# Kernel optimization log

Hardware: AMD Instinct MI355X
Metric: run time of the kernel (lower is better)

Reference implementation:

```python
import jax, jax.numpy as jnp
import numpy as np

B, E, N, F = 8, 2048, 2048, 128

def setup_inputs() -> dict:
    key = jax.random.key(0)
    k1, k2, k3, k4 = jax.random.split(key, 4)
    node_embeddings = jax.random.normal(k1, (B, N, F), dtype=jnp.float32)
    adj = jax.random.randint(k2, (B, E, N), -1, 3).astype(jnp.float32)
    W = jax.random.normal(k3, (F, F), dtype=jnp.float32) * (1.0 / np.sqrt(F))
    b = jax.random.normal(k4, (F,), dtype=jnp.float32) * 0.01
    return {"node_embeddings": node_embeddings, "adj": adj, "W": W, "b": b}

def reference(node_embeddings, adj, W, b):
    # adj_target: 1 where adj == -1, else 0
    adj_target = (adj == -1).astype(node_embeddings.dtype)          # [B, E, N]
    norm = jnp.sum(adj_target, axis=-1, keepdims=True)               # [B, E, 1]
    norm = jnp.where(norm == 0, 1.0, norm)
    # masked-mean aggregation of neighbor vertices into hyperedges
    message_vertex = jnp.matmul(adj_target, node_embeddings) / norm  # [B, E, F]
    # linear (torch Linear: x @ W.T + b) + relu
    hyperedge_embeddings = jax.nn.relu(jnp.matmul(message_vertex, W.T) + b)
    return hyperedge_embeddings
```

## Files before the change

### kernel.cpp

```cpp
#include <hip/hip_runtime.h>
#include <hip/hip_bf16.h>

#define B_ 8
#define E_ 2048
#define N_ 2048
#define F_ 128

#define BM 64
#define MT 4
#define BK 64
#define MP 136

using bf16x8 = __bf16 __attribute__((ext_vector_type(8)));
using fx4    = float __attribute__((ext_vector_type(4)));

__global__ __launch_bounds__(256) void prep_all(const float* __restrict__ node,
                                                const float* __restrict__ W,
                                                __bf16* __restrict__ nodeT,
                                                __bf16* __restrict__ Wb) {
    const int bid = blockIdx.x;
    const int t   = threadIdx.x;

    if (bid < 512) {
        const int b  = bid & 7;
        const int n0 = (bid >> 3) * 32;
        const int f  = t & 127;
        const int nb = n0 + (t >> 7) * 16;
        const float* src = node + ((size_t)b * N_ + nb) * F_ + f;
        __bf16 h[16];
#pragma unroll
        for (int i = 0; i < 16; ++i)
            h[i] = (__bf16)src[(size_t)i * F_];
        __bf16* dst = nodeT + ((size_t)b * F_ + f) * N_ + nb;
        *(uint4*)&dst[0] = *(const uint4*)&h[0];
        *(uint4*)&dst[8] = *(const uint4*)&h[8];
    } else {
        int idx = (bid - 512) * 256 + t;
        float4 v = *(const float4*)&W[idx * 4];
        __bf16 o[4] = {(__bf16)v.x, (__bf16)v.y, (__bf16)v.z, (__bf16)v.w};
        *(uint2*)&Wb[idx * 4] = *(const uint2*)o;
    }
}

__global__ __launch_bounds__(256, 1) void v2h_main(const float* __restrict__ adj,
                                                   const __bf16* __restrict__ nodeT,
                                                   const __bf16* __restrict__ Wb,
                                                   const float* __restrict__ bias,
                                                   float* __restrict__ out) {
    __shared__ __align__(16) __bf16 Bs[2][128][64];
    __shared__ __align__(16) unsigned long long Abits[2][64];
    __shared__ __align__(16) float normS[BM];
    __shared__ __align__(16) __bf16 Ms[BM * MP];

    const int t    = threadIdx.x;
    const int bid  = blockIdx.x;
    const int b    = bid & 7;
    const int e0   = (bid >> 3) * BM;
    const int w    = t >> 6;
    const int lane = t & 63;
    const int l15  = lane & 15;
    const int quad = lane >> 4;

    const int ar   = lane >> 2;
    const int acs  = lane & 3;
    const int arow = w * 16 + ar;
    const float* aPtr = adj + ((size_t)b * E_ + e0 + arow) * N_ + acs * 16;

    const __bf16* nTB = nodeT + (size_t)b * F_ * N_;

    auto issue_dma = [&](int k0, int buf) {
#pragma unroll
        for (int p = 0; p < 4; ++p) {
            int idx = t + 256 * p;
            int f   = idx >> 3;
            int sl  = idx & 7;
            int g   = sl ^ (f & 7);
            const __bf16* src = nTB + (size_t)f * N_ + k0 + g * 8;
            __bf16* dst = &Bs[buf][0][0] + (size_t)(w * 64 + 256 * p) * 8;
            __builtin_amdgcn_global_load_lds(
                (const __attribute__((address_space(1))) void*)src,
                (__attribute__((address_space(3))) void*)dst, 16, 0, 0);
        }
    };

    auto cvt16 = [](float4 v0, float4 v1, float4 v2, float4 v3) -> unsigned {
        unsigned m = 0;
        m |= (v0.x == -1.f) ? 1u     : 0u;
        m |= (v0.y == -1.f) ? 2u     : 0u;
        m |= (v0.z == -1.f) ? 4u     : 0u;
        m |= (v0.w == -1.f) ? 8u     : 0u;
        m |= (v1.x == -1.f) ? 16u    : 0u;
        m |= (v1.y == -1.f) ? 32u    : 0u;
        m |= (v1.z == -1.f) ? 64u    : 0u;
        m |= (v1.w == -1.f) ? 128u   : 0u;
        m |= (v2.x == -1.f) ? 256u   : 0u;
        m |= (v2.y == -1.f) ? 512u   : 0u;
        m |= (v2.z == -1.f) ? 1024u  : 0u;
        m |= (v2.w == -1.f) ? 2048u  : 0u;
        m |= (v3.x == -1.f) ? 4096u  : 0u;
        m |= (v3.y == -1.f) ? 8192u  : 0u;
        m |= (v3.z == -1.f) ? 16384u : 0u;
        m |= (v3.w == -1.f) ? 32768u : 0u;
        return m;
    };

    auto unpack = [](unsigned byte) -> bf16x8 {
        union { unsigned u[4]; bf16x8 v; } r;
        r.u[0] = ((byte &   1u) ? 0x3F80u : 0u) | ((byte &   2u) ? 0x3F800000u : 0u);
        r.u[1] = ((byte &   4u) ? 0x3F80u : 0u) | ((byte &   8u) ? 0x3F800000u : 0u);
        r.u[2] = ((byte &  16u) ? 0x3F80u : 0u) | ((byte &  32u) ? 0x3F800000u : 0u);
        r.u[3] = ((byte &  64u) ? 0x3F80u : 0u) | ((byte & 128u) ? 0x3F800000u : 0u);
        return r.v;
    };

    fx4 acc[MT][2] = {};
    int cnt = 0;

    float4 a0 = *(const float4*)(aPtr + 0);
    float4 a1 = *(const float4*)(aPtr + 4);
    float4 a2 = *(const float4*)(aPtr + 8);
    float4 a3 = *(const float4*)(aPtr + 12);
    issue_dma(0, 0);
    {
        unsigned bits = cvt16(a0, a1, a2, a3);
        ((unsigned short*)&Abits[0][arow])[acs] = (unsigned short)bits;
        cnt += __popc(bits);
    }
    a0 = *(const float4*)(aPtr + BK + 0);
    a1 = *(const float4*)(aPtr + BK + 4);
    a2 = *(const float4*)(aPtr + BK + 8);
    a3 = *(const float4*)(aPtr + BK + 12);

#pragma unroll
    for (int m = 0; m < 32; ++m) {
        const int buf = m & 1;
        __syncthreads();

        if (m < 31)
            issue_dma((m + 1) * BK, buf ^ 1);
        if (m < 31) {
            unsigned bits = cvt16(a0, a1, a2, a3);
            ((unsigned short*)&Abits[buf ^ 1][arow])[acs] = (unsigned short)bits;
            cnt += __popc(bits);
        }
        if (m < 30) {
            const float* ap = aPtr + (m + 2) * BK;
            a0 = *(const float4*)(ap + 0);
            a1 = *(const float4*)(ap + 4);
            a2 = *(const float4*)(ap + 8);
            a3 = *(const float4*)(ap + 12);
        }

        bf16x8 af0[MT], af1[MT];
#pragma unroll
        for (int mt = 0; mt < MT; ++mt) {
            unsigned long long v = Abits[buf][mt * 16 + l15];
            unsigned lo = (unsigned)v, hi = (unsigned)(v >> 32);
            af0[mt] = unpack((lo >> (8 * quad)) & 255u);
            af1[mt] = unpack((hi >> (8 * quad)) & 255u);
        }

#pragma unroll
        for (int ft = 0; ft < 2; ++ft) {
            int f  = w * 32 + ft * 16 + l15;
            int q0 = quad ^ (f & 7);
            int q1 = (4 + quad) ^ (f & 7);
            bf16x8 b0 = *(const bf16x8*)&Bs[buf][f][q0 * 8];
#pragma unroll
            for (int mt = 0; mt < MT; ++mt)
                acc[mt][ft] = __builtin_amdgcn_mfma_f32_16x16x32_bf16(af0[mt], b0, acc[mt][ft], 0, 0, 0);
            bf16x8 b1 = *(const bf16x8*)&Bs[buf][f][q1 * 8];
#pragma unroll
            for (int mt = 0; mt < MT; ++mt)
                acc[mt][ft] = __builtin_amdgcn_mfma_f32_16x16x32_bf16(af1[mt], b1, acc[mt][ft], 0, 0, 0);
        }
    }

    {
        float c = (float)cnt;
        c += __shfl_xor(c, 1);
        c += __shfl_xor(c, 2);
        if (acs == 0)
            normS[arow] = 1.f / fmaxf(c, 1.f);
    }
    __syncthreads();

    const int rbase = quad * 4;
    float4 rn[MT];
#pragma unroll
    for (int mt = 0; mt < MT; ++mt)
        rn[mt] = *(const float4*)&normS[mt * 16 + rbase];

#pragma unroll
    for (int ft = 0; ft < 2; ++ft) {
        int fcol = w * 32 + ft * 16 + l15;
#pragma unroll
        for (int mt = 0; mt < MT; ++mt) {
            const float* rr = (const float*)&rn[mt];
#pragma unroll
            for (int r = 0; r < 4; ++r)
                Ms[(mt * 16 + rbase + r) * MP + fcol] = (__bf16)(acc[mt][ft][r] * rr[r]);
        }
    }
    __syncthreads();

    fx4 acc2[MT][2] = {};
#pragma unroll
    for (int ks = 0; ks < 4; ++ks) {
        bf16x8 afm[MT];
#pragma unroll
        for (int mt = 0; mt < MT; ++mt)
            afm[mt] = *(const bf16x8*)&Ms[(mt * 16 + l15) * MP + ks * 32 + quad * 8];
#pragma unroll
        for (int gt = 0; gt < 2; ++gt) {
            int g = w * 32 + gt * 16 + l15;
            bf16x8 wfr = *(const bf16x8*)&Wb[(size_t)g * F_ + ks * 32 + quad * 8];
#pragma unroll
            for (int mt = 0; mt < MT; ++mt)
                acc2[mt][gt] = __builtin_amdgcn_mfma_f32_16x16x32_bf16(afm[mt], wfr, acc2[mt][gt], 0, 0, 0);
        }
    }

#pragma unroll
    for (int gt = 0; gt < 2; ++gt) {
        int g = w * 32 + gt * 16 + l15;
        float bb = bias[g];
#pragma unroll
        for (int mt = 0; mt < MT; ++mt) {
#pragma unroll
            for (int r = 0; r < 4; ++r) {
                int e = e0 + mt * 16 + rbase + r;
                float v = acc2[mt][gt][r] + bb;
                out[((size_t)b * E_ + e) * F_ + g] = fmaxf(v, 0.f);
            }
        }
    }
}

extern "C" void kernel_launch(void* const* d_in, const int* in_sizes, int n_in,
                              void* d_out, int out_size, void* d_ws, size_t ws_size,
                              hipStream_t stream) {
    const float* node = (const float*)d_in[0];
    const float* adj  = (const float*)d_in[1];
    const float* W    = (const float*)d_in[2];
    const float* bias = (const float*)d_in[3];
    float* out = (float*)d_out;

    char* ws = (char*)d_ws;
    __bf16* nodeT = (__bf16*)ws;
    __bf16* Wb    = (__bf16*)(ws + 8 * 1024 * 1024);

    prep_all<<<528, 256, 0, stream>>>(node, W, nodeT, Wb);
    v2h_main<<<256, 256, 0, stream>>>(adj, nodeT, Wb, bias, out);
}
```

Before: 210.6 us.

## Fuse node/W bf16 prep into main kernel with per-batch flag synchronization

Removes the separate prep kernel. Each of the 256 blocks now transposes and converts its own 64-node slice of its batch's node embeddings, and 16 blocks also convert W. Readiness is published through atomic flags in workspace. The K loop starts at the block's own slice and rotates through the rest, spin-waiting on a flag only when it reaches a slice that is not yet ready. The aim is to cut the launch gap and overlap prep with compute. In exchange it adds a memset, spin-wait overhead, and a reliance on all 256 blocks being co-resident, since otherwise the waits can deadlock.

Measured after the change: 282.1 us. 1.34x slower.

```diff
diff --git a/kernel.cpp b/kernel.cpp
--- a/kernel.cpp
+++ b/kernel.cpp
@@ -14,39 +14,14 @@
 using bf16x8 = __bf16 __attribute__((ext_vector_type(8)));
 using fx4    = float __attribute__((ext_vector_type(4)));
 
-__global__ __launch_bounds__(256) void prep_all(const float* __restrict__ node,
-                                                const float* __restrict__ W,
-                                                __bf16* __restrict__ nodeT,
-                                                __bf16* __restrict__ Wb) {
-    const int bid = blockIdx.x;
-    const int t   = threadIdx.x;
-
-    if (bid < 512) {
-        const int b  = bid & 7;
-        const int n0 = (bid >> 3) * 32;
-        const int f  = t & 127;
-        const int nb = n0 + (t >> 7) * 16;
-        const float* src = node + ((size_t)b * N_ + nb) * F_ + f;
-        __bf16 h[16];
-#pragma unroll
-        for (int i = 0; i < 16; ++i)
-            h[i] = (__bf16)src[(size_t)i * F_];
-        __bf16* dst = nodeT + ((size_t)b * F_ + f) * N_ + nb;
-        *(uint4*)&dst[0] = *(const uint4*)&h[0];
-        *(uint4*)&dst[8] = *(const uint4*)&h[8];
-    } else {
-        int idx = (bid - 512) * 256 + t;
-        float4 v = *(const float4*)&W[idx * 4];
-        __bf16 o[4] = {(__bf16)v.x, (__bf16)v.y, (__bf16)v.z, (__bf16)v.w};
-        *(uint2*)&Wb[idx * 4] = *(const uint2*)o;
-    }
-}
-
-__global__ __launch_bounds__(256, 1) void v2h_main(const float* __restrict__ adj,
-                                                   const __bf16* __restrict__ nodeT,
-                                                   const __bf16* __restrict__ Wb,
-                                                   const float* __restrict__ bias,
-                                                   float* __restrict__ out) {
+__global__ __launch_bounds__(256, 1) void v2h_fused(const float* __restrict__ node,
+                                                    const float* __restrict__ adj,
+                                                    const float* __restrict__ W,
+                                                    const float* __restrict__ bias,
+                                                    __bf16* __restrict__ nodeT,
+                                                    __bf16* __restrict__ Wb,
+                                                    unsigned* __restrict__ flags,
+                                                    float* __restrict__ out) {
     __shared__ __align__(16) __bf16 Bs[2][128][64];
     __shared__ __align__(16) unsigned long long Abits[2][64];
     __shared__ __align__(16) float normS[BM];
@@ -55,17 +30,47 @@
     const int t    = threadIdx.x;
     const int bid  = blockIdx.x;
     const int b    = bid & 7;
-    const int e0   = (bid >> 3) * BM;
+    const int j    = bid >> 3;
+    const int e0   = j * BM;
     const int w    = t >> 6;
     const int lane = t & 63;
     const int l15  = lane & 15;
     const int quad = lane >> 4;
 
+    {
+        const int f = t & 127;
+#pragma unroll
+        for (int u = 0; u < 2; ++u) {
+            const int nb = j * 64 + u * 32 + (t >> 7) * 16;
+            const float* src = node + ((size_t)b * N_ + nb) * F_ + f;
+            __bf16 h[16];
+#pragma unroll
+            for (int i = 0; i < 16; ++i)
+                h[i] = (__bf16)src[(size_t)i * F_];
+            __bf16* dst = nodeT + ((size_t)b * F_ + f) * N_ + nb;
+            *(uint4*)&dst[0] = *(const uint4*)&h[0];
+            *(uint4*)&dst[8] = *(const uint4*)&h[8];
+        }
+    }
+    __syncthreads();
+    if (t == 0) {
+        __threadfence();
+        atomicOr(&flags[b], 1u << j);
+    }
+
+    if (bid < 16) {
+        int idx = bid * 256 + t;
+        float4 v = *(const float4*)&W[idx * 4];
+        __bf16 o[4] = {(__bf16)v.x, (__bf16)v.y, (__bf16)v.z, (__bf16)v.w};
+        *(uint2*)&Wb[idx * 4] = *(const uint2*)o;
+        __syncthreads();
+        if (t == 0) { __threadfence(); atomicAdd(&flags[8], 1u); }
+    }
+
     const int ar   = lane >> 2;
     const int acs  = lane & 3;
     const int arow = w * 16 + ar;
-    const float* aPtr = adj + ((size_t)b * E_ + e0 + arow) * N_ + acs * 16;
-
+    const float* aRow = adj + ((size_t)b * E_ + e0 + arow) * N_ + acs * 16;
     const __bf16* nTB = nodeT + (size_t)b * F_ * N_;
 
     auto issue_dma = [&](int k0, int buf) {
@@ -115,36 +120,48 @@
 
     fx4 acc[MT][2] = {};
     int cnt = 0;
-
-    float4 a0 = *(const float4*)(aPtr + 0);
-    float4 a1 = *(const float4*)(aPtr + 4);
-    float4 a2 = *(const float4*)(aPtr + 8);
-    float4 a3 = *(const float4*)(aPtr + 12);
-    issue_dma(0, 0);
+    unsigned seen = 1u << j;
+
+    float4 a0 = *(const float4*)(aRow + j * BK + 0);
+    float4 a1 = *(const float4*)(aRow + j * BK + 4);
+    float4 a2 = *(const float4*)(aRow + j * BK + 8);
+    float4 a3 = *(const float4*)(aRow + j * BK + 12);
+    issue_dma(j * BK, 0);
     {
         unsigned bits = cvt16(a0, a1, a2, a3);
         ((unsigned short*)&Abits[0][arow])[acs] = (unsigned short)bits;
         cnt += __popc(bits);
     }
-    a0 = *(const float4*)(aPtr + BK + 0);
-    a1 = *(const float4*)(aPtr + BK + 4);
-    a2 = *(const float4*)(aPtr + BK + 8);
-    a3 = *(const float4*)(aPtr + BK + 12);
+    {
+        const float* ap = aRow + (((j + 1) & 31) * BK);
+        a0 = *(const float4*)(ap + 0);
+        a1 = *(const float4*)(ap + 4);
+        a2 = *(const float4*)(ap + 8);
+        a3 = *(const float4*)(ap + 12);
+    }
 
 #pragma unroll
     for (int m = 0; m < 32; ++m) {
         const int buf = m & 1;
+        const int ktn = (m + 1 + j) & 31;
+
+        if (m < 31 && t == 0 && !((seen >> ktn) & 1)) {
+            unsigned msk;
+            while (!(((msk = atomicOr(&flags[b], 0u)) >> ktn) & 1))
+                __builtin_amdgcn_s_sleep(8);
+            seen |= msk;
+            __threadfence();
+        }
         __syncthreads();
 
-        if (m < 31)
-            issue_dma((m + 1) * BK, buf ^ 1);
         if (m < 31) {
+            issue_dma(ktn * BK, buf ^ 1);
             unsigned bits = cvt16(a0, a1, a2, a3);
             ((unsigned short*)&Abits[buf ^ 1][arow])[acs] = (unsigned short)bits;
             cnt += __popc(bits);
         }
         if (m < 30) {
-            const float* ap = aPtr + (m + 2) * BK;
+            const float* ap = aRow + (((m + 2 + j) & 31) * BK);
             a0 = *(const float4*)(ap + 0);
             a1 = *(const float4*)(ap + 4);
             a2 = *(const float4*)(ap + 8);
@@ -201,6 +218,11 @@
             for (int r = 0; r < 4; ++r)
                 Ms[(mt * 16 + rbase + r) * MP + fcol] = (__bf16)(acc[mt][ft][r] * rr[r]);
         }
+    }
+    if (t == 0) {
+        while (atomicAdd(&flags[8], 0u) < 16u)
+            __builtin_amdgcn_s_sleep(8);
+        __threadfence();
     }
     __syncthreads();
 
@@ -247,9 +269,10 @@
     float* out = (float*)d_out;
 
     char* ws = (char*)d_ws;
-    __bf16* nodeT = (__bf16*)ws;
-    __bf16* Wb    = (__bf16*)(ws + 8 * 1024 * 1024);
-
-    prep_all<<<528, 256, 0, stream>>>(node, W, nodeT, Wb);
-    v2h_main<<<256, 256, 0, stream>>>(adj, nodeT, Wb, bias, out);
+    __bf16*   nodeT = (__bf16*)ws;
+    __bf16*   Wb    = (__bf16*)(ws + 8 * 1024 * 1024);
+    unsigned* flags = (unsigned*)(ws + 8 * 1024 * 1024 + 65536);
+
+    hipMemsetAsync(flags, 0, 64, stream);
+    v2h_fused<<<256, 256, 0, stream>>>(node, adj, W, bias, nodeT, Wb, flags, out);
 }
```

## Fuse bf16 prep into main kernel, loading fp32 node tiles directly into LDS

Applied to the files above, without the earlier changes.

Drops the separate prep kernel that transposed the node embeddings and converted them and W to bf16. The main kernel now DMAs fp32 node rows straight into a rotated-swizzled LDS tile and converts to bf16 while building the MFMA B fragments with strided scalar LDS reads. W is converted on the fly from fp32 global loads. This removes one launch and the extra global write and read of nodeT, at the cost of twice the LDS traffic per tile, eight scalar LDS loads per fragment instead of one vector load, and more conversion ALU work in the inner loop.

After: 231.6 us. 10.0% more time.

```diff
diff --git a/kernel.cpp b/kernel.cpp
--- a/kernel.cpp
+++ b/kernel.cpp
@@ -14,42 +14,14 @@
 using bf16x8 = __bf16 __attribute__((ext_vector_type(8)));
 using fx4    = float __attribute__((ext_vector_type(4)));
 
-__global__ __launch_bounds__(256) void prep_all(const float* __restrict__ node,
-                                                const float* __restrict__ W,
-                                                __bf16* __restrict__ nodeT,
-                                                __bf16* __restrict__ Wb) {
-    const int bid = blockIdx.x;
-    const int t   = threadIdx.x;
-
-    if (bid < 512) {
-        const int b  = bid & 7;
-        const int n0 = (bid >> 3) * 32;
-        const int f  = t & 127;
-        const int nb = n0 + (t >> 7) * 16;
-        const float* src = node + ((size_t)b * N_ + nb) * F_ + f;
-        __bf16 h[16];
-#pragma unroll
-        for (int i = 0; i < 16; ++i)
-            h[i] = (__bf16)src[(size_t)i * F_];
-        __bf16* dst = nodeT + ((size_t)b * F_ + f) * N_ + nb;
-        *(uint4*)&dst[0] = *(const uint4*)&h[0];
-        *(uint4*)&dst[8] = *(const uint4*)&h[8];
-    } else {
-        int idx = (bid - 512) * 256 + t;
-        float4 v = *(const float4*)&W[idx * 4];
-        __bf16 o[4] = {(__bf16)v.x, (__bf16)v.y, (__bf16)v.z, (__bf16)v.w};
-        *(uint2*)&Wb[idx * 4] = *(const uint2*)o;
-    }
-}
-
 __global__ __launch_bounds__(256, 1) void v2h_main(const float* __restrict__ adj,
-                                                   const __bf16* __restrict__ nodeT,
-                                                   const __bf16* __restrict__ Wb,
+                                                   const float* __restrict__ node,
+                                                   const float* __restrict__ W,
                                                    const float* __restrict__ bias,
                                                    float* __restrict__ out) {
-    __shared__ __align__(16) __bf16 Bs[2][128][64];
+    __shared__ __align__(16) float Bs[2][64][128];
     __shared__ __align__(16) unsigned long long Abits[2][64];
-    __shared__ __align__(16) float normS[BM];
+    __shared__ float normS[BM];
     __shared__ __align__(16) __bf16 Ms[BM * MP];
 
     const int t    = threadIdx.x;
@@ -64,19 +36,18 @@
     const int ar   = lane >> 2;
     const int acs  = lane & 3;
     const int arow = w * 16 + ar;
-    const float* aPtr = adj + ((size_t)b * E_ + e0 + arow) * N_ + acs * 16;
-
-    const __bf16* nTB = nodeT + (size_t)b * F_ * N_;
+    const float* aRow = adj + ((size_t)b * E_ + e0 + arow) * N_ + acs * 16;
+    const float* nB   = node + (size_t)b * N_ * F_;
 
     auto issue_dma = [&](int k0, int buf) {
 #pragma unroll
-        for (int p = 0; p < 4; ++p) {
+        for (int p = 0; p < 8; ++p) {
             int idx = t + 256 * p;
-            int f   = idx >> 3;
-            int sl  = idx & 7;
-            int g   = sl ^ (f & 7);
-            const __bf16* src = nTB + (size_t)f * N_ + k0 + g * 8;
-            __bf16* dst = &Bs[buf][0][0] + (size_t)(w * 64 + 256 * p) * 8;
+            int n   = idx >> 5;
+            int sl  = idx & 31;
+            int fs  = (sl - 2 * ((n >> 3) & 3)) & 31;
+            const float* src = nB + (size_t)(k0 + n) * F_ + fs * 4;
+            float* dst = &Bs[buf][0][0] + (size_t)(w * 64 + 256 * p) * 4;
             __builtin_amdgcn_global_load_lds(
                 (const __attribute__((address_space(1))) void*)src,
                 (__attribute__((address_space(3))) void*)dst, 16, 0, 0);
@@ -113,38 +84,44 @@
         return r.v;
     };
 
+    int colf[2];
+#pragma unroll
+    for (int ft = 0; ft < 2; ++ft) {
+        int f = w * 32 + ft * 16 + l15;
+        colf[ft] = (((f >> 2) + 2 * quad) & 31) * 4 + (f & 3);
+    }
+
     fx4 acc[MT][2] = {};
     int cnt = 0;
 
-    float4 a0 = *(const float4*)(aPtr + 0);
-    float4 a1 = *(const float4*)(aPtr + 4);
-    float4 a2 = *(const float4*)(aPtr + 8);
-    float4 a3 = *(const float4*)(aPtr + 12);
+    float4 a0 = *(const float4*)(aRow + 0);
+    float4 a1 = *(const float4*)(aRow + 4);
+    float4 a2 = *(const float4*)(aRow + 8);
+    float4 a3 = *(const float4*)(aRow + 12);
     issue_dma(0, 0);
     {
         unsigned bits = cvt16(a0, a1, a2, a3);
         ((unsigned short*)&Abits[0][arow])[acs] = (unsigned short)bits;
         cnt += __popc(bits);
     }
-    a0 = *(const float4*)(aPtr + BK + 0);
-    a1 = *(const float4*)(aPtr + BK + 4);
-    a2 = *(const float4*)(aPtr + BK + 8);
-    a3 = *(const float4*)(aPtr + BK + 12);
+    a0 = *(const float4*)(aRow + BK + 0);
+    a1 = *(const float4*)(aRow + BK + 4);
+    a2 = *(const float4*)(aRow + BK + 8);
+    a3 = *(const float4*)(aRow + BK + 12);
 
 #pragma unroll
     for (int m = 0; m < 32; ++m) {
         const int buf = m & 1;
         __syncthreads();
 
-        if (m < 31)
+        if (m < 31) {
             issue_dma((m + 1) * BK, buf ^ 1);
-        if (m < 31) {
             unsigned bits = cvt16(a0, a1, a2, a3);
             ((unsigned short*)&Abits[buf ^ 1][arow])[acs] = (unsigned short)bits;
             cnt += __popc(bits);
         }
         if (m < 30) {
-            const float* ap = aPtr + (m + 2) * BK;
+            const float* ap = aRow + (m + 2) * BK;
             a0 = *(const float4*)(ap + 0);
             a1 = *(const float4*)(ap + 4);
             a2 = *(const float4*)(ap + 8);
@@ -162,14 +139,20 @@
 
 #pragma unroll
         for (int ft = 0; ft < 2; ++ft) {
-            int f  = w * 32 + ft * 16 + l15;
-            int q0 = quad ^ (f & 7);
-            int q1 = (4 + quad) ^ (f & 7);
-            bf16x8 b0 = *(const bf16x8*)&Bs[buf][f][q0 * 8];
+            bf16x8 b0, b1;
+            {
+                const float* bp = &Bs[buf][quad * 8][0] + colf[ft];
+#pragma unroll
+                for (int jj = 0; jj < 8; ++jj) b0[jj] = (__bf16)bp[jj * 128];
+            }
+            {
+                const float* bp = &Bs[buf][(4 + quad) * 8][0] + colf[ft];
+#pragma unroll
+                for (int jj = 0; jj < 8; ++jj) b1[jj] = (__bf16)bp[jj * 128];
+            }
 #pragma unroll
             for (int mt = 0; mt < MT; ++mt)
                 acc[mt][ft] = __builtin_amdgcn_mfma_f32_16x16x32_bf16(af0[mt], b0, acc[mt][ft], 0, 0, 0);
-            bf16x8 b1 = *(const bf16x8*)&Bs[buf][f][q1 * 8];
 #pragma unroll
             for (int mt = 0; mt < MT; ++mt)
                 acc[mt][ft] = __builtin_amdgcn_mfma_f32_16x16x32_bf16(af1[mt], b1, acc[mt][ft], 0, 0, 0);
@@ -214,7 +197,14 @@
 #pragma unroll
         for (int gt = 0; gt < 2; ++gt) {
             int g = w * 32 + gt * 16 + l15;
-            bf16x8 wfr = *(const bf16x8*)&Wb[(size_t)g * F_ + ks * 32 + quad * 8];
+            const float* wp = W + (size_t)g * F_ + ks * 32 + quad * 8;
+            float4 wa = *(const float4*)wp;
+            float4 wb = *(const float4*)(wp + 4);
+            bf16x8 wfr;
+            wfr[0] = (__bf16)wa.x; wfr[1] = (__bf16)wa.y;
+            wfr[2] = (__bf16)wa.z; wfr[3] = (__bf16)wa.w;
+            wfr[4] = (__bf16)wb.x; wfr[5] = (__bf16)wb.y;
+            wfr[6] = (__bf16)wb.z; wfr[7] = (__bf16)wb.w;
 #pragma unroll
             for (int mt = 0; mt < MT; ++mt)
                 acc2[mt][gt] = __builtin_amdgcn_mfma_f32_16x16x32_bf16(afm[mt], wfr, acc2[mt][gt], 0, 0, 0);
@@ -246,10 +236,5 @@
     const float* bias = (const float*)d_in[3];
     float* out = (float*)d_out;
 
-    char* ws = (char*)d_ws;
-    __bf16* nodeT = (__bf16*)ws;
-    __bf16* Wb    = (__bf16*)(ws + 8 * 1024 * 1024);
-
-    prep_all<<<528, 256, 0, stream>>>(node, W, nodeT, Wb);
-    v2h_main<<<256, 256, 0, stream>>>(adj, nodeT, Wb, bias, out);
+    v2h_main<<<256, 256, 0, stream>>>(adj, node, W, bias, out);
 }
```

## Halve edge tile to 32 rows, launch 512 blocks, convert W in-kernel

Applied to the files above, without the earlier changes.

Shrinks the per-block hyperedge tile from 64 to 32 rows, so the main kernel runs 512 blocks and allows two blocks per CU. The adjacency-load mapping changes to 8 threads per row with 8 floats each. W is now read as fp32 and converted to bf16 inside the second GEMM, which removes the W prep pass from the first kernel. The cost is that each block now loads the full nodeT tile for only half as many rows, roughly doubling B-operand traffic and per-row MFMA efficiency loss.

Result: slower. 221.6 us (+5.3%).

```diff
diff --git a/kernel.cpp b/kernel.cpp
--- a/kernel.cpp
+++ b/kernel.cpp
@@ -6,50 +6,42 @@
 #define N_ 2048
 #define F_ 128
 
-#define BM 64
-#define MT 4
+#define BM 32
+#define MT 2
 #define BK 64
 #define MP 136
 
 using bf16x8 = __bf16 __attribute__((ext_vector_type(8)));
 using fx4    = float __attribute__((ext_vector_type(4)));
 
-__global__ __launch_bounds__(256) void prep_all(const float* __restrict__ node,
-                                                const float* __restrict__ W,
-                                                __bf16* __restrict__ nodeT,
-                                                __bf16* __restrict__ Wb) {
+__global__ __launch_bounds__(256) void prep_node(const float* __restrict__ node,
+                                                 __bf16* __restrict__ nodeT) {
     const int bid = blockIdx.x;
+    const int b   = bid & 7;
+    const int n0  = (bid >> 3) * 32;
     const int t   = threadIdx.x;
-
-    if (bid < 512) {
-        const int b  = bid & 7;
-        const int n0 = (bid >> 3) * 32;
-        const int f  = t & 127;
-        const int nb = n0 + (t >> 7) * 16;
-        const float* src = node + ((size_t)b * N_ + nb) * F_ + f;
-        __bf16 h[16];
-#pragma unroll
-        for (int i = 0; i < 16; ++i)
-            h[i] = (__bf16)src[(size_t)i * F_];
-        __bf16* dst = nodeT + ((size_t)b * F_ + f) * N_ + nb;
-        *(uint4*)&dst[0] = *(const uint4*)&h[0];
-        *(uint4*)&dst[8] = *(const uint4*)&h[8];
-    } else {
-        int idx = (bid - 512) * 256 + t;
-        float4 v = *(const float4*)&W[idx * 4];
-        __bf16 o[4] = {(__bf16)v.x, (__bf16)v.y, (__bf16)v.z, (__bf16)v.w};
-        *(uint2*)&Wb[idx * 4] = *(const uint2*)o;
-    }
+    const int f   = t & 127;
+    const int nb  = n0 + (t >> 7) * 16;
+
+    const float* src = node + ((size_t)b * N_ + nb) * F_ + f;
+    __bf16 h[16];
+#pragma unroll
+    for (int i = 0; i < 16; ++i)
+        h[i] = (__bf16)src[(size_t)i * F_];
+
+    __bf16* dst = nodeT + ((size_t)b * F_ + f) * N_ + nb;
+    *(uint4*)&dst[0] = *(const uint4*)&h[0];
+    *(uint4*)&dst[8] = *(const uint4*)&h[8];
 }
 
-__global__ __launch_bounds__(256, 1) void v2h_main(const float* __restrict__ adj,
+__global__ __launch_bounds__(256, 2) void v2h_main(const float* __restrict__ adj,
                                                    const __bf16* __restrict__ nodeT,
-                                                   const __bf16* __restrict__ Wb,
+                                                   const float* __restrict__ W,
                                                    const float* __restrict__ bias,
                                                    float* __restrict__ out) {
     __shared__ __align__(16) __bf16 Bs[2][128][64];
-    __shared__ __align__(16) unsigned long long Abits[2][64];
-    __shared__ __align__(16) float normS[BM];
+    __shared__ __align__(16) unsigned long long Abits[2][BM];
+    __shared__ float normS[BM];
     __shared__ __align__(16) __bf16 Ms[BM * MP];
 
     const int t    = threadIdx.x;
@@ -61,11 +53,9 @@
     const int l15  = lane & 15;
     const int quad = lane >> 4;
 
-    const int ar   = lane >> 2;
-    const int acs  = lane & 3;
-    const int arow = w * 16 + ar;
-    const float* aPtr = adj + ((size_t)b * E_ + e0 + arow) * N_ + acs * 16;
-
+    const int ar  = t >> 3;
+    const int acs = t & 7;
+    const float* aRow = adj + ((size_t)b * E_ + e0 + ar) * N_ + acs * 8;
     const __bf16* nTB = nodeT + (size_t)b * F_ * N_;
 
     auto issue_dma = [&](int k0, int buf) {
@@ -83,24 +73,16 @@
         }
     };
 
-    auto cvt16 = [](float4 v0, float4 v1, float4 v2, float4 v3) -> unsigned {
+    auto cvt8 = [](float4 v0, float4 v1) -> unsigned {
         unsigned m = 0;
-        m |= (v0.x == -1.f) ? 1u     : 0u;
-        m |= (v0.y == -1.f) ? 2u     : 0u;
-        m |= (v0.z == -1.f) ? 4u     : 0u;
-        m |= (v0.w == -1.f) ? 8u     : 0u;
-        m |= (v1.x == -1.f) ? 16u    : 0u;
-        m |= (v1.y == -1.f) ? 32u    : 0u;
-        m |= (v1.z == -1.f) ? 64u    : 0u;
-        m |= (v1.w == -1.f) ? 128u   : 0u;
-        m |= (v2.x == -1.f) ? 256u   : 0u;
-        m |= (v2.y == -1.f) ? 512u   : 0u;
-        m |= (v2.z == -1.f) ? 1024u  : 0u;
-        m |= (v2.w == -1.f) ? 2048u  : 0u;
-        m |= (v3.x == -1.f) ? 4096u  : 0u;
-        m |= (v3.y == -1.f) ? 8192u  : 0u;
-        m |= (v3.z == -1.f) ? 16384u : 0u;
-        m |= (v3.w == -1.f) ? 32768u : 0u;
+        m |= (v0.x == -1.f) ? 1u   : 0u;
+        m |= (v0.y == -1.f) ? 2u   : 0u;
+        m |= (v0.z == -1.f) ? 4u   : 0u;
+        m |= (v0.w == -1.f) ? 8u   : 0u;
+        m |= (v1.x == -1.f) ? 16u  : 0u;
+        m |= (v1.y == -1.f) ? 32u  : 0u;
+        m |= (v1.z == -1.f) ? 64u  : 0u;
+        m |= (v1.w == -1.f) ? 128u : 0u;
         return m;
     };
 
@@ -116,39 +98,32 @@
     fx4 acc[MT][2] = {};
     int cnt = 0;
 
-    float4 a0 = *(const float4*)(aPtr + 0);
-    float4 a1 = *(const float4*)(aPtr + 4);
-    float4 a2 = *(const float4*)(aPtr + 8);
-    float4 a3 = *(const float4*)(aPtr + 12);
+    float4 a0 = *(const float4*)(aRow + 0);
+    float4 a1 = *(const float4*)(aRow + 4);
     issue_dma(0, 0);
     {
-        unsigned bits = cvt16(a0, a1, a2, a3);
-        ((unsigned short*)&Abits[0][arow])[acs] = (unsigned short)bits;
+        unsigned bits = cvt8(a0, a1);
+        ((unsigned char*)&Abits[0][ar])[acs] = (unsigned char)bits;
         cnt += __popc(bits);
     }
-    a0 = *(const float4*)(aPtr + BK + 0);
-    a1 = *(const float4*)(aPtr + BK + 4);
-    a2 = *(const float4*)(aPtr + BK + 8);
-    a3 = *(const float4*)(aPtr + BK + 12);
+    a0 = *(const float4*)(aRow + BK + 0);
+    a1 = *(const float4*)(aRow + BK + 4);
 
 #pragma unroll
     for (int m = 0; m < 32; ++m) {
         const int buf = m & 1;
         __syncthreads();
 
-        if (m < 31)
+        if (m < 31) {
             issue_dma((m + 1) * BK, buf ^ 1);
-        if (m < 31) {
-            unsigned bits = cvt16(a0, a1, a2, a3);
-            ((unsigned short*)&Abits[buf ^ 1][arow])[acs] = (unsigned short)bits;
+            unsigned bits = cvt8(a0, a1);
+            ((unsigned char*)&Abits[buf ^ 1][ar])[acs] = (unsigned char)bits;
             cnt += __popc(bits);
         }
         if (m < 30) {
-            const float* ap = aPtr + (m + 2) * BK;
+            const float* ap = aRow + (m + 2) * BK;
             a0 = *(const float4*)(ap + 0);
             a1 = *(const float4*)(ap + 4);
-            a2 = *(const float4*)(ap + 8);
-            a3 = *(const float4*)(ap + 12);
         }
 
         bf16x8 af0[MT], af1[MT];
@@ -180,8 +155,9 @@
         float c = (float)cnt;
         c += __shfl_xor(c, 1);
         c += __shfl_xor(c, 2);
+        c += __shfl_xor(c, 4);
         if (acs == 0)
-            normS[arow] = 1.f / fmaxf(c, 1.f);
+            normS[ar] = 1.f / fmaxf(c, 1.f);
     }
     __syncthreads();
 
@@ -214,7 +190,14 @@
 #pragma unroll
         for (int gt = 0; gt < 2; ++gt) {
             int g = w * 32 + gt * 16 + l15;
-            bf16x8 wfr = *(const bf16x8*)&Wb[(size_t)g * F_ + ks * 32 + quad * 8];
+            const float* wp = W + (size_t)g * F_ + ks * 32 + quad * 8;
+            float4 wa = *(const float4*)wp;
+            float4 wb = *(const float4*)(wp + 4);
+            bf16x8 wfr;
+            wfr[0] = (__bf16)wa.x; wfr[1] = (__bf16)wa.y;
+            wfr[2] = (__bf16)wa.z; wfr[3] = (__bf16)wa.w;
+            wfr[4] = (__bf16)wb.x; wfr[5] = (__bf16)wb.y;
+            wfr[6] = (__bf16)wb.z; wfr[7] = (__bf16)wb.w;
 #pragma unroll
             for (int mt = 0; mt < MT; ++mt)
                 acc2[mt][gt] = __builtin_amdgcn_mfma_f32_16x16x32_bf16(afm[mt], wfr, acc2[mt][gt], 0, 0, 0);
@@ -246,10 +229,8 @@
     const float* bias = (const float*)d_in[3];
     float* out = (float*)d_out;
 
-    char* ws = (char*)d_ws;
-    __bf16* nodeT = (__bf16*)ws;
-    __bf16* Wb    = (__bf16*)(ws + 8 * 1024 * 1024);
-
-    prep_all<<<528, 256, 0, stream>>>(node, W, nodeT, Wb);
-    v2h_main<<<256, 256, 0, stream>>>(adj, nodeT, Wb, bias, out);
+    __bf16* nodeT = (__bf16*)d_ws;
+
+    prep_node<<<512, 256, 0, stream>>>(node, nodeT);
+    v2h_main<<<512, 256, 0, stream>>>(adj, nodeT, W, bias, out);
 }
```
